# Kernel optimization log

Hardware: AMD Instinct MI355X
Metric: run time of the kernel (lower is better)

Reference implementation:

```python
import jax, jax.numpy as jnp
import numpy as np

N = 100000      # nodes
E = 400000      # edges
DIN, DH, DOUT = 32, 128, 1
EPS = 1e-5


def _lin_init(key, fan_in, shape):
    s = 1.0 / np.sqrt(fan_in)
    return jax.random.uniform(key, shape, jnp.float32, -s, s)


def setup_inputs() -> dict:
    key = jax.random.key(0)
    ks = jax.random.split(key, 24)
    x = jax.random.normal(ks[0], (N, DIN), jnp.float32)
    edge_index = jax.random.randint(ks[1], (2, E), 0, N, dtype=jnp.int64)
    d = {"x": x, "edge_index": edge_index}
    dims = [(DIN, DH), (DH, DH), (DH, DOUT)]
    for i, (din, dout) in enumerate(dims, start=1):
        d[f"W{i}"] = _lin_init(ks[2 * i], din, (din, dout))
        d[f"b{i}"] = _lin_init(ks[2 * i + 1], din, (dout,))
        d[f"g{i}"] = jnp.ones((dout,), jnp.float32)    # BatchNorm weight
        d[f"bt{i}"] = jnp.zeros((dout,), jnp.float32)  # BatchNorm bias
        d[f"lw{i}"] = jnp.ones((dout,), jnp.float32)   # LayerNorm weight
        d[f"lb{i}"] = jnp.zeros((dout,), jnp.float32)  # LayerNorm bias
    return d


def reference(x, edge_index, W1, b1, g1, bt1, lw1, lb1,
              W2, b2, g2, bt2, lw2, lb2,
              W3, b3, g3, bt3, lw3, lb3):
    n = x.shape[0]
    loop = jnp.arange(n, dtype=edge_index.dtype)
    src = jnp.concatenate([edge_index[0], loop])  # self-loops added (GCNConv default)
    dst = jnp.concatenate([edge_index[1], loop])
    deg = jax.ops.segment_sum(jnp.ones(src.shape[0], x.dtype), dst, num_segments=n)
    dinv = jnp.where(deg > 0, jax.lax.rsqrt(deg), 0.0)
    norm = dinv[src] * dinv[dst]  # D^{-1/2} (A+I) D^{-1/2} edge weights

    def gcn(h, W, b):
        h = h @ W
        agg = jax.ops.segment_sum(h[src] * norm[:, None], dst, num_segments=n)
        return agg + b

    def bn(h, g, b):  # BatchNorm1d, training-mode batch stats (biased var)
        m = h.mean(0)
        v = h.var(0)
        return (h - m) * jax.lax.rsqrt(v + EPS) * g + b

    def inorm(h):  # PyG InstanceNorm, single graph, affine=False
        m = h.mean(0)
        v = h.var(0)
        return (h - m) * jax.lax.rsqrt(v + EPS)

    def lnorm(h, w, b):  # PyG LayerNorm, mode='graph': stats over all nodes+channels
        m = h.mean()
        v = h.var()
        return (h - m) * jax.lax.rsqrt(v + EPS) * w + b

    h = jax.nn.relu(lnorm(inorm(bn(gcn(x, W1, b1), g1, bt1)), lw1, lb1))
    h = jax.nn.relu(lnorm(inorm(bn(gcn(h, W2, b2), g2, bt2)), lw2, lb2))
    h = lnorm(inorm(bn(gcn(h, W3, b3), g3, bt3)), lw3, lb3)
    return h.flatten()
```

## Files before the change

kernel.cpp:

```cpp
#include <hip/hip_runtime.h>
#include <cstddef>

#define EPS 1e-5f

typedef __attribute__((ext_vector_type(8))) short bf16x8;
typedef __attribute__((ext_vector_type(8))) unsigned short u16x8;
typedef __attribute__((ext_vector_type(4))) float f32x4;

__device__ inline short f2bf(float f) {
    union { float f; unsigned u; } v;
    v.f = f;
    unsigned r = v.u + 0x7fff + ((v.u >> 16) & 1);
    return (short)(r >> 16);
}
__device__ inline float bf2f(unsigned short s) {
    union { unsigned u; float f; } v;
    v.u = ((unsigned)s) << 16;
    return v.f;
}

__global__ void hist_kernel(const int* __restrict__ dst, int E, int* __restrict__ counts) {
    int i = blockIdx.x * blockDim.x + threadIdx.x;
    if (i < E) atomicAdd(&counts[dst[i]], 1);
}

__global__ __launch_bounds__(1024) void scan_part(const int* __restrict__ counts,
                                                  int* __restrict__ rowptr,
                                                  int* __restrict__ aux, int n) {
    __shared__ int sh[1024];
    int t = threadIdx.x;
    int g = blockIdx.x * 1024 + t;
    int v = (g < n) ? counts[g] : 0;
    sh[t] = v;
    __syncthreads();
    for (int off = 1; off < 1024; off <<= 1) {
        int add = (t >= off) ? sh[t - off] : 0;
        __syncthreads();
        sh[t] += add;
        __syncthreads();
    }
    if (g < n) rowptr[g] = sh[t] - v;
    if (t == 1023) aux[blockIdx.x] = sh[t];
}

__global__ __launch_bounds__(128) void scan_aux(int* __restrict__ aux, int B) {
    __shared__ int sh[128];
    int t = threadIdx.x;
    int v = (t < B) ? aux[t] : 0;
    sh[t] = v;
    __syncthreads();
    for (int off = 1; off < 128; off <<= 1) {
        int add = (t >= off) ? sh[t - off] : 0;
        __syncthreads();
        sh[t] += add;
        __syncthreads();
    }
    if (t < B) aux[t] = sh[t] - v;
}

__global__ void scan_add(int* __restrict__ rowptr, const int* __restrict__ aux,
                         const int* __restrict__ counts, int* __restrict__ cur,
                         float* __restrict__ dinv, int n, int E) {
    int g = blockIdx.x * blockDim.x + threadIdx.x;
    if (g < n) {
        int r = rowptr[g] + aux[g >> 10];
        rowptr[g] = r;
        cur[g] = r;
        dinv[g] = rsqrtf((float)counts[g] + 1.0f);
    }
    if (g == 0) rowptr[n] = E;
}

__global__ void fill_kernel(const int* __restrict__ src, const int* __restrict__ dst, int E,
                            int* __restrict__ cur, const float* __restrict__ dinv,
                            int* __restrict__ esrc, float* __restrict__ ewt) {
    int e = blockIdx.x * blockDim.x + threadIdx.x;
    if (e < E) {
        int d = dst[e];
        int s = src[e];
        int p = atomicAdd(&cur[d], 1);
        esrc[p] = s;
        ewt[p] = dinv[s] * dinv[d];
    }
}

__global__ void wt_all_kernel(const float* __restrict__ W1, const float* __restrict__ W2,
                              unsigned short* __restrict__ Wt1, unsigned short* __restrict__ Wt2) {
    int o = blockIdx.x * blockDim.x + threadIdx.x;
    if (o < 32 * 128) {
        int c = o / 32, k = o % 32;
        Wt1[o] = (unsigned short)f2bf(W1[(size_t)k * 128 + c]);
    } else if (o < 32 * 128 + 128 * 128) {
        int o2 = o - 32 * 128;
        int c = o2 / 128, k = o2 % 128;
        Wt2[o2] = (unsigned short)f2bf(W2[(size_t)k * 128 + c]);
    }
}

template <int K, bool NORM, bool STATS>
__global__ __launch_bounds__(256) void gemm_mfma(const unsigned short* __restrict__ hb,
                                                 const unsigned short* __restrict__ Wt,
                                                 const float* __restrict__ ss,
                                                 unsigned short* __restrict__ outb,
                                                 float* __restrict__ sums, int n) {
    int wid = (blockIdx.x * 256 + threadIdx.x) >> 6;
    int wv = (threadIdx.x >> 6);
    int lane = threadIdx.x & 63;
    int m = lane & 15;
    int qd = lane >> 4;
    int r0 = wid * 32;
    if (!STATS && r0 >= n) return;

    f32x4 acc[2][8];
#pragma unroll
    for (int rt = 0; rt < 2; rt++)
#pragma unroll
        for (int ct = 0; ct < 8; ct++) acc[rt][ct] = (f32x4){0.f, 0.f, 0.f, 0.f};

    if (r0 < n) {
#pragma unroll
        for (int q = 0; q < K / 32; q++) {
            int k0 = q * 32 + qd * 8;
            bf16x8 a[2];
#pragma unroll
            for (int rt = 0; rt < 2; rt++) {
                int r = r0 + rt * 16 + m;
                bf16x8 av = (bf16x8){0, 0, 0, 0, 0, 0, 0, 0};
                if (r < n) av = *(const bf16x8*)(hb + (size_t)r * K + k0);
                if (NORM) {
#pragma unroll
                    for (int j = 0; j < 8; j++) {
                        float f = bf2f((unsigned short)av[j]);
                        f = fmaxf(fmaf(f, ss[k0 + j], ss[K + k0 + j]), 0.f);
                        av[j] = f2bf(f);
                    }
                }
                a[rt] = av;
            }
#pragma unroll
            for (int ct = 0; ct < 8; ct++) {
                bf16x8 b = *(const bf16x8*)(Wt + (size_t)(ct * 16 + m) * K + k0);
                acc[0][ct] = __builtin_amdgcn_mfma_f32_16x16x32_bf16(a[0], b, acc[0][ct], 0, 0, 0);
                acc[1][ct] = __builtin_amdgcn_mfma_f32_16x16x32_bf16(a[1], b, acc[1][ct], 0, 0, 0);
            }
        }
#pragma unroll
        for (int rt = 0; rt < 2; rt++)
#pragma unroll
            for (int i = 0; i < 4; i++) {
                int r = r0 + rt * 16 + qd * 4 + i;
                if (r < n) {
#pragma unroll
                    for (int ct = 0; ct < 8; ct++)
                        outb[(size_t)r * 128 + ct * 16 + m] = (unsigned short)f2bf(acc[rt][ct][i]);
                }
            }
    }

    if (STATS) {
        __shared__ float ls[4][128], lq[4][128];
#pragma unroll
        for (int ct = 0; ct < 8; ct++) {
            float s = 0.f, q = 0.f;
#pragma unroll
            for (int rt = 0; rt < 2; rt++)
#pragma unroll
                for (int i = 0; i < 4; i++) {
                    float v = acc[rt][ct][i];
                    s += v;
                    q += v * v;
                }
            s += __shfl_xor(s, 16, 64);
            s += __shfl_xor(s, 32, 64);
            q += __shfl_xor(q, 16, 64);
            q += __shfl_xor(q, 32, 64);
            if (qd == 0) {
                ls[wv][ct * 16 + m] = s;
                lq[wv][ct * 16 + m] = q;
            }
        }
        __syncthreads();
        int t = threadIdx.x;
        if (t < 128) {
            atomicAdd(&sums[t], ls[0][t] + ls[1][t] + ls[2][t] + ls[3][t]);
        } else {
            int c = t - 128;
            atomicAdd(&sums[128 + c], lq[0][c] + lq[1][c] + lq[2][c] + lq[3][c]);
        }
    }
}

__global__ void gemv_norm_bf(const unsigned short* __restrict__ hb, const float* __restrict__ W,
                             const float* __restrict__ ss, float* __restrict__ out, int n) {
    int gid = blockIdx.x * blockDim.x + threadIdx.x;
    int wid = gid >> 6, lane = gid & 63;
    int nw = (gridDim.x * blockDim.x) >> 6;
    int c = lane * 2;
    float w0 = W[c], w1 = W[c + 1];
    float s0 = ss[c], s1 = ss[c + 1];
    float t0 = ss[128 + c], t1 = ss[128 + c + 1];
    for (int r = wid; r < n; r += nw) {
        ushort2 u = ((const ushort2*)(hb + (size_t)r * 128))[lane];
        float a = fmaxf(fmaf(bf2f(u.x), s0, t0), 0.f);
        float b = fmaxf(fmaf(bf2f(u.y), s1, t1), 0.f);
        float v = fmaf(a, w0, b * w1);
#pragma unroll
        for (int off = 32; off > 0; off >>= 1) v += __shfl_down(v, off, 64);
        if (lane == 0) out[r] = v;
    }
}

__global__ __launch_bounds__(256) void agg128_bf(const unsigned short* __restrict__ tmp,
                                                 const int* __restrict__ rowptr,
                                                 const int* __restrict__ esrc,
                                                 const float* __restrict__ ewt,
                                                 const float* __restrict__ dinv,
                                                 unsigned short* __restrict__ agg, int n) {
    int node = (blockIdx.x << 3) + (threadIdx.x >> 5);
    if (node >= n) return;
    int c4 = threadIdx.x & 31;
    float di = dinv[node];
    float d2 = di * di;
    ushort4 t = ((const ushort4*)tmp)[(size_t)node * 32 + c4];
    float a0 = bf2f(t.x) * d2, a1 = bf2f(t.y) * d2, a2 = bf2f(t.z) * d2, a3 = bf2f(t.w) * d2;
    int j = rowptr[node], je = rowptr[node + 1];
    for (; j + 8 <= je; j += 8) {
        int s[8];
        float w[8];
        ushort4 v[8];
#pragma unroll
        for (int k = 0; k < 8; k++) { s[k] = esrc[j + k]; w[k] = ewt[j + k]; }
#pragma unroll
        for (int k = 0; k < 8; k++) v[k] = ((const ushort4*)tmp)[(size_t)s[k] * 32 + c4];
#pragma unroll
        for (int k = 0; k < 8; k++) {
            a0 = fmaf(bf2f(v[k].x), w[k], a0);
            a1 = fmaf(bf2f(v[k].y), w[k], a1);
            a2 = fmaf(bf2f(v[k].z), w[k], a2);
            a3 = fmaf(bf2f(v[k].w), w[k], a3);
        }
    }
    if (j + 4 <= je) {
        int s[4];
        float w[4];
        ushort4 v[4];
#pragma unroll
        for (int k = 0; k < 4; k++) { s[k] = esrc[j + k]; w[k] = ewt[j + k]; }
#pragma unroll
        for (int k = 0; k < 4; k++) v[k] = ((const ushort4*)tmp)[(size_t)s[k] * 32 + c4];
#pragma unroll
        for (int k = 0; k < 4; k++) {
            a0 = fmaf(bf2f(v[k].x), w[k], a0);
            a1 = fmaf(bf2f(v[k].y), w[k], a1);
            a2 = fmaf(bf2f(v[k].z), w[k], a2);
            a3 = fmaf(bf2f(v[k].w), w[k], a3);
        }
        j += 4;
    }
    for (; j < je; j++) {
        int s = esrc[j];
        float w = ewt[j];
        ushort4 v = ((const ushort4*)tmp)[(size_t)s * 32 + c4];
        a0 = fmaf(bf2f(v.x), w, a0);
        a1 = fmaf(bf2f(v.y), w, a1);
        a2 = fmaf(bf2f(v.z), w, a2);
        a3 = fmaf(bf2f(v.w), w, a3);
    }
    ushort4 o;
    o.x = (unsigned short)f2bf(a0);
    o.y = (unsigned short)f2bf(a1);
    o.z = (unsigned short)f2bf(a2);
    o.w = (unsigned short)f2bf(a3);
    ((ushort4*)agg)[(size_t)node * 32 + c4] = o;
}

__global__ __launch_bounds__(256) void stats128_bf(const unsigned short* __restrict__ a,
                                                   float* __restrict__ sums, int n) {
    __shared__ float ls[16][128], lq[16][128];
    int t = threadIdx.x;
    int rg = t >> 4;
    int cg = t & 15;
    float s[8], q[8];
#pragma unroll
    for (int k = 0; k < 8; k++) { s[k] = 0.f; q[k] = 0.f; }
    for (int r = blockIdx.x * 16 + rg; r < n; r += gridDim.x * 16) {
        u16x8 v = *(const u16x8*)(a + (size_t)r * 128 + cg * 8);
#pragma unroll
        for (int k = 0; k < 8; k++) {
            float f = bf2f(v[k]);
            s[k] += f;
            q[k] = fmaf(f, f, q[k]);
        }
    }
#pragma unroll
    for (int k = 0; k < 8; k++) {
        ls[rg][cg * 8 + k] = s[k];
        lq[rg][cg * 8 + k] = q[k];
    }
    __syncthreads();
    if (t < 128) {
        float v = 0.f;
#pragma unroll
        for (int i = 0; i < 16; i++) v += ls[i][t];
        atomicAdd(&sums[t], v);
    } else {
        int c = t - 128;
        float v = 0.f;
#pragma unroll
        for (int i = 0; i < 16; i++) v += lq[i][c];
        atomicAdd(&sums[128 + c], v);
    }
}

__global__ __launch_bounds__(256) void agg32_f(const float* __restrict__ x,
                                               const int* __restrict__ rowptr,
                                               const int* __restrict__ esrc,
                                               const float* __restrict__ ewt,
                                               const float* __restrict__ dinv,
                                               unsigned short* __restrict__ xab, int n) {
    int g = threadIdx.x >> 3;
    int lane = threadIdx.x & 7;
    int node = blockIdx.x * 32 + g;
    if (node >= n) return;
    int co = lane << 2;
    float di = dinv[node];
    float d2 = di * di;
    float4 a = *(const float4*)(x + ((size_t)node << 5) + co);
    a.x *= d2; a.y *= d2; a.z *= d2; a.w *= d2;
    int j = rowptr[node], je = rowptr[node + 1];
    for (; j + 4 <= je; j += 4) {
        int s0 = esrc[j], s1 = esrc[j + 1], s2 = esrc[j + 2], s3 = esrc[j + 3];
        float w0 = ewt[j], w1 = ewt[j + 1], w2 = ewt[j + 2], w3 = ewt[j + 3];
        float4 v0 = *(const float4*)(x + ((size_t)s0 << 5) + co);
        float4 v1 = *(const float4*)(x + ((size_t)s1 << 5) + co);
        float4 v2 = *(const float4*)(x + ((size_t)s2 << 5) + co);
        float4 v3 = *(const float4*)(x + ((size_t)s3 << 5) + co);
        a.x = fmaf(v0.x, w0, a.x); a.y = fmaf(v0.y, w0, a.y);
        a.z = fmaf(v0.z, w0, a.z); a.w = fmaf(v0.w, w0, a.w);
        a.x = fmaf(v1.x, w1, a.x); a.y = fmaf(v1.y, w1, a.y);
        a.z = fmaf(v1.z, w1, a.z); a.w = fmaf(v1.w, w1, a.w);
        a.x = fmaf(v2.x, w2, a.x); a.y = fmaf(v2.y, w2, a.y);
        a.z = fmaf(v2.z, w2, a.z); a.w = fmaf(v2.w, w2, a.w);
        a.x = fmaf(v3.x, w3, a.x); a.y = fmaf(v3.y, w3, a.y);
        a.z = fmaf(v3.z, w3, a.z); a.w = fmaf(v3.w, w3, a.w);
    }
    for (; j < je; j++) {
        int s = esrc[j];
        float w = ewt[j];
        float4 v = *(const float4*)(x + ((size_t)s << 5) + co);
        a.x = fmaf(v.x, w, a.x); a.y = fmaf(v.y, w, a.y);
        a.z = fmaf(v.z, w, a.z); a.w = fmaf(v.w, w, a.w);
    }
    ushort4 o;
    o.x = (unsigned short)f2bf(a.x);
    o.y = (unsigned short)f2bf(a.y);
    o.z = (unsigned short)f2bf(a.z);
    o.w = (unsigned short)f2bf(a.w);
    ((ushort4*)(xab + ((size_t)node << 5)))[lane] = o;
}

__global__ void agg1_stats(const float* __restrict__ tmp, const int* __restrict__ rowptr,
                           const int* __restrict__ esrc, const float* __restrict__ ewt,
                           const float* __restrict__ dinv, float* __restrict__ out,
                           float* __restrict__ part, int n) {
    int i = blockIdx.x * blockDim.x + threadIdx.x;
    float acc = 0.f;
    if (i < n) {
        float di = dinv[i];
        acc = tmp[i] * di * di;
        int j = rowptr[i], je = rowptr[i + 1];
        for (; j + 4 <= je; j += 4) {
            int s0 = esrc[j], s1 = esrc[j + 1], s2 = esrc[j + 2], s3 = esrc[j + 3];
            float w0 = ewt[j], w1 = ewt[j + 1], w2 = ewt[j + 2], w3 = ewt[j + 3];
            float v0 = tmp[s0], v1 = tmp[s1], v2 = tmp[s2], v3 = tmp[s3];
            acc = fmaf(v0, w0, acc);
            acc = fmaf(v1, w1, acc);
            acc = fmaf(v2, w2, acc);
            acc = fmaf(v3, w3, acc);
        }
        for (; j < je; j++) acc = fmaf(tmp[esrc[j]], ewt[j], acc);
        out[i] = acc;
    }
    float s = acc, q = acc * acc;
#pragma unroll
    for (int off = 32; off > 0; off >>= 1) {
        s += __shfl_down(s, off, 64);
        q += __shfl_down(q, off, 64);
    }
    if ((threadIdx.x & 63) == 0) {
        int wgid = (blockIdx.x * blockDim.x + threadIdx.x) >> 6;
        part[2 * wgid] = s;
        part[2 * wgid + 1] = q;
    }
}

__global__ __launch_bounds__(256) void reduce_part(const float* __restrict__ part,
                                                   float* __restrict__ sums, int nw) {
    __shared__ float ls[256], lq[256];
    int t = threadIdx.x;
    float s = 0.f, q = 0.f;
    for (int i = t; i < nw; i += 256) {
        s += part[2 * i];
        q += part[2 * i + 1];
    }
    ls[t] = s;
    lq[t] = q;
    __syncthreads();
    for (int off = 128; off > 0; off >>= 1) {
        if (t < off) {
            ls[t] += ls[t + off];
            lq[t] += lq[t + off];
        }
        __syncthreads();
    }
    if (t == 0) {
        sums[0] = ls[0];
        sums[1] = lq[0];
    }
}

__global__ void apply1_kernel(const float* __restrict__ sums, const float* __restrict__ g,
                              const float* __restrict__ lw, const float* __restrict__ lb,
                              const float* __restrict__ a, float* __restrict__ out, int n) {
    int i = blockIdx.x * blockDim.x + threadIdx.x;
    if (i >= n) return;
    float m = sums[0] / n;
    float v = sums[1] / n - m * m;
    v = v < 0.f ? 0.f : v;
    float bs = rsqrtf(v + EPS) * g[0];
    float vz = v * bs * bs;
    float t = bs * rsqrtf(vz + EPS);
    float GV = v * t * t;
    float S = t * rsqrtf(GV + EPS) * lw[0];
    float T = lb[0] - m * S;
    out[i] = fmaf(a[i], S, T);
}

template <int C>
__global__ void finalize_kernel(const float* __restrict__ sums, const float* __restrict__ g,
                                const float* __restrict__ lw, const float* __restrict__ lb,
                                float* __restrict__ ss, int n) {
    __shared__ float vt2[C];
    int c = threadIdx.x;
    float m = sums[c] / n;
    float v = sums[C + c] / n - m * m;
    v = v < 0.f ? 0.f : v;
    float gc = g[c];
    float bs = rsqrtf(v + EPS) * gc;
    float vz = v * bs * bs;
    float t = bs * rsqrtf(vz + EPS);
    vt2[c] = v * t * t;
    __syncthreads();
    if (c == 0) {
        float gv = 0.f;
        for (int i = 0; i < C; i++) gv += vt2[i];
        vt2[0] = gv / C;
    }
    __syncthreads();
    float GV = vt2[0];
    float S = t * rsqrtf(GV + EPS) * lw[c];
    ss[c] = S;
    ss[C + c] = lb[c] - m * S;
}

extern "C" void kernel_launch(void* const* d_in, const int* in_sizes, int n_in,
                              void* d_out, int out_size, void* d_ws, size_t ws_size,
                              hipStream_t stream) {
    const float* x = (const float*)d_in[0];
    const int* ei = (const int*)d_in[1];
    int n = in_sizes[0] / 32;
    int E = in_sizes[1] / 2;
    const int* src = ei;
    const int* dstp = ei + E;
    const float* W1 = (const float*)d_in[2];
    const float* g1 = (const float*)d_in[4];
    const float* lw1 = (const float*)d_in[6];
    const float* lb1 = (const float*)d_in[7];
    const float* W2 = (const float*)d_in[8];
    const float* g2 = (const float*)d_in[10];
    const float* lw2 = (const float*)d_in[12];
    const float* lb2 = (const float*)d_in[13];
    const float* W3 = (const float*)d_in[14];
    const float* g3 = (const float*)d_in[16];
    const float* lw3 = (const float*)d_in[18];
    const float* lb3 = (const float*)d_in[19];
    float* out = (float*)d_out;

    char* p = (char*)d_ws;
    int* counts = (int*)p;             p += (size_t)n * 4;
    int* cur = (int*)p;                p += (size_t)n * 4;
    int* rowptr = (int*)p;             p += (size_t)(n + 4) * 4;
    int* aux = (int*)p;                p += 128 * 4;
    int* esrc = (int*)p;               p += (size_t)E * 4;
    float* ewt = (float*)p;            p += (size_t)E * 4;
    float* dinv = (float*)p;           p += (size_t)n * 4;
    unsigned short* Wt1 = (unsigned short*)p;  p += 128 * 32 * 2;
    unsigned short* Wt2 = (unsigned short*)p;  p += 128 * 128 * 2;
    unsigned short* xa = (unsigned short*)p;   p += (size_t)n * 32 * 2;
    unsigned short* h1 = (unsigned short*)p;   p += (size_t)n * 128 * 2;
    unsigned short* t2 = (unsigned short*)p;   p += (size_t)n * 128 * 2;
    unsigned short* a2 = (unsigned short*)p;   p += (size_t)n * 128 * 2;
    float* t3 = (float*)p;             p += (size_t)n * 4;
    float* a3 = (float*)p;             p += (size_t)n * 4;
    float* sums1 = (float*)p;          p += 256 * 4;
    float* sums2 = (float*)p;          p += 256 * 4;
    float* sums3 = (float*)p;          p += 4 * 4;
    float* ss1 = (float*)p;            p += 256 * 4;
    float* ss2 = (float*)p;            p += 256 * 4;
    float* part3 = (float*)p;          p += ((size_t)(n + 255) / 256) * 4 * 2 * 4;

    int B = (n + 1023) / 1024;

    hipMemsetAsync(counts, 0, (size_t)n * 4, stream);
    hipMemsetAsync(sums1, 0, 516 * 4, stream);
    hist_kernel<<<(E + 255) / 256, 256, 0, stream>>>(dstp, E, counts);
    scan_part<<<B, 1024, 0, stream>>>(counts, rowptr, aux, n);
    scan_aux<<<1, 128, 0, stream>>>(aux, B);
    scan_add<<<(n + 255) / 256, 256, 0, stream>>>(rowptr, aux, counts, cur, dinv, n, E);
    fill_kernel<<<(E + 255) / 256, 256, 0, stream>>>(src, dstp, E, cur, dinv, esrc, ewt);
    wt_all_kernel<<<(32 * 128 + 128 * 128 + 255) / 256, 256, 0, stream>>>(W1, W2, Wt1, Wt2);

    int mblk = ((n + 31) / 32 + 3) / 4;

    agg32_f<<<(n + 31) / 32, 256, 0, stream>>>(x, rowptr, esrc, ewt, dinv, xa, n);
    gemm_mfma<32, false, true><<<mblk, 256, 0, stream>>>(xa, Wt1, nullptr, h1, sums1, n);
    finalize_kernel<128><<<1, 128, 0, stream>>>(sums1, g1, lw1, lb1, ss1, n);

    gemm_mfma<128, true, false><<<mblk, 256, 0, stream>>>(h1, Wt2, ss1, t2, nullptr, n);
    agg128_bf<<<(n + 7) / 8, 256, 0, stream>>>(t2, rowptr, esrc, ewt, dinv, a2, n);
    stats128_bf<<<512, 256, 0, stream>>>(a2, sums2, n);
    finalize_kernel<128><<<1, 128, 0, stream>>>(sums2, g2, lw2, lb2, ss2, n);

    int ablk1 = (n + 255) / 256;
    gemv_norm_bf<<<1024, 256, 0, stream>>>(a2, W3, ss2, t3, n);
    agg1_stats<<<ablk1, 256, 0, stream>>>(t3, rowptr, esrc, ewt, dinv, a3, part3, n);
    reduce_part<<<1, 256, 0, stream>>>(part3, sums3, ablk1 * 4);
    apply1_kernel<<<(n + 255) / 256, 256, 0, stream>>>(sums3, g3, lw3, lb3, a3, out, n);
}
```

Before: 311.0 us.

## Fuse setup kernels, use decoupled-lookback scan, widen agg128 loads to 16B

```diff
diff --git a/kernel.cpp b/kernel.cpp
--- a/kernel.cpp
+++ b/kernel.cpp
@@ -19,17 +19,44 @@
     return v.f;
 }
 
+__global__ void prep_kernel(const float* __restrict__ W1, const float* __restrict__ W2,
+                            unsigned short* __restrict__ Wt1, unsigned short* __restrict__ Wt2,
+                            int* __restrict__ counts, float* __restrict__ sums,
+                            unsigned long long* __restrict__ state, int* __restrict__ ticket,
+                            int n) {
+    int o = blockIdx.x * blockDim.x + threadIdx.x;
+    if (o < n) counts[o] = 0;
+    if (o < 516) sums[o] = 0.f;
+    if (o < 128) state[o] = 0ULL;
+    if (o == 0) *ticket = 0;
+    if (o < 32 * 128) {
+        int c = o / 32, k = o % 32;
+        Wt1[o] = (unsigned short)f2bf(W1[(size_t)k * 128 + c]);
+    } else if (o < 32 * 128 + 128 * 128) {
+        int o2 = o - 32 * 128;
+        int c = o2 / 128, k = o2 % 128;
+        Wt2[o2] = (unsigned short)f2bf(W2[(size_t)k * 128 + c]);
+    }
+}
+
 __global__ void hist_kernel(const int* __restrict__ dst, int E, int* __restrict__ counts) {
     int i = blockIdx.x * blockDim.x + threadIdx.x;
     if (i < E) atomicAdd(&counts[dst[i]], 1);
 }
 
-__global__ __launch_bounds__(1024) void scan_part(const int* __restrict__ counts,
-                                                  int* __restrict__ rowptr,
-                                                  int* __restrict__ aux, int n) {
+__global__ __launch_bounds__(1024) void scan_lookback(const int* __restrict__ counts,
+                                                      int* __restrict__ rowptr,
+                                                      int* __restrict__ cur,
+                                                      float* __restrict__ dinv,
+                                                      unsigned long long* __restrict__ state,
+                                                      int* __restrict__ ticket, int n, int E) {
     __shared__ int sh[1024];
+    __shared__ int sbid, sexcl;
     int t = threadIdx.x;
-    int g = blockIdx.x * 1024 + t;
+    if (t == 0) sbid = atomicAdd(ticket, 1);
+    __syncthreads();
+    int bid = sbid;
+    int g = bid * 1024 + t;
     int v = (g < n) ? counts[g] : 0;
     sh[t] = v;
     __syncthreads();
@@ -39,31 +66,30 @@
         sh[t] += add;
         __syncthreads();
     }
-    if (g < n) rowptr[g] = sh[t] - v;
-    if (t == 1023) aux[blockIdx.x] = sh[t];
-}
-
-__global__ __launch_bounds__(128) void scan_aux(int* __restrict__ aux, int B) {
-    __shared__ int sh[128];
-    int t = threadIdx.x;
-    int v = (t < B) ? aux[t] : 0;
-    sh[t] = v;
-    __syncthreads();
-    for (int off = 1; off < 128; off <<= 1) {
-        int add = (t >= off) ? sh[t - off] : 0;
-        __syncthreads();
-        sh[t] += add;
-        __syncthreads();
-    }
-    if (t < B) aux[t] = sh[t] - v;
-}
-
-__global__ void scan_add(int* __restrict__ rowptr, const int* __restrict__ aux,
-                         const int* __restrict__ counts, int* __restrict__ cur,
-                         float* __restrict__ dinv, int n, int E) {
-    int g = blockIdx.x * blockDim.x + threadIdx.x;
+    int total = sh[1023];
+    if (t == 0) {
+        if (bid == 0) {
+            atomicExch(&state[0], (2ULL << 32) | (unsigned)total);
+            sexcl = 0;
+        } else {
+            atomicExch(&state[bid], (1ULL << 32) | (unsigned)total);
+            int excl = 0;
+            int j = bid - 1;
+            while (true) {
+                unsigned long long s;
+                do { s = atomicAdd(&state[j], 0ULL); } while ((s >> 32) == 0);
+                excl += (int)(s & 0xffffffffULL);
+                if ((s >> 32) == 2ULL) break;
+                j--;
+            }
+            atomicExch(&state[bid], (2ULL << 32) | (unsigned)(excl + total));
+            sexcl = excl;
+        }
+    }
+    __syncthreads();
+    int excl = sexcl;
     if (g < n) {
-        int r = rowptr[g] + aux[g >> 10];
+        int r = excl + sh[t] - v;
         rowptr[g] = r;
         cur[g] = r;
         dinv[g] = rsqrtf((float)counts[g] + 1.0f);
@@ -81,19 +107,6 @@
         int p = atomicAdd(&cur[d], 1);
         esrc[p] = s;
         ewt[p] = dinv[s] * dinv[d];
-    }
-}
-
-__global__ void wt_all_kernel(const float* __restrict__ W1, const float* __restrict__ W2,
-                              unsigned short* __restrict__ Wt1, unsigned short* __restrict__ Wt2) {
-    int o = blockIdx.x * blockDim.x + threadIdx.x;
-    if (o < 32 * 128) {
-        int c = o / 32, k = o % 32;
-        Wt1[o] = (unsigned short)f2bf(W1[(size_t)k * 128 + c]);
-    } else if (o < 32 * 128 + 128 * 128) {
-        int o2 = o - 32 * 128;
-        int c = o2 / 128, k = o2 % 128;
-        Wt2[o2] = (unsigned short)f2bf(W2[(size_t)k * 128 + c]);
     }
 }
 
@@ -216,62 +229,54 @@
                                                  const float* __restrict__ ewt,
                                                  const float* __restrict__ dinv,
                                                  unsigned short* __restrict__ agg, int n) {
-    int node = (blockIdx.x << 3) + (threadIdx.x >> 5);
+    int node = (blockIdx.x << 4) + (threadIdx.x >> 4);
     if (node >= n) return;
-    int c4 = threadIdx.x & 31;
+    int co = (threadIdx.x & 15) << 3;
     float di = dinv[node];
     float d2 = di * di;
-    ushort4 t = ((const ushort4*)tmp)[(size_t)node * 32 + c4];
-    float a0 = bf2f(t.x) * d2, a1 = bf2f(t.y) * d2, a2 = bf2f(t.z) * d2, a3 = bf2f(t.w) * d2;
+    u16x8 t = *(const u16x8*)(tmp + ((size_t)node << 7) + co);
+    float acc[8];
+#pragma unroll
+    for (int k = 0; k < 8; k++) acc[k] = bf2f(t[k]) * d2;
     int j = rowptr[node], je = rowptr[node + 1];
     for (; j + 8 <= je; j += 8) {
         int s[8];
         float w[8];
-        ushort4 v[8];
+        u16x8 v[8];
 #pragma unroll
         for (int k = 0; k < 8; k++) { s[k] = esrc[j + k]; w[k] = ewt[j + k]; }
 #pragma unroll
-        for (int k = 0; k < 8; k++) v[k] = ((const ushort4*)tmp)[(size_t)s[k] * 32 + c4];
-#pragma unroll
-        for (int k = 0; k < 8; k++) {
-            a0 = fmaf(bf2f(v[k].x), w[k], a0);
-            a1 = fmaf(bf2f(v[k].y), w[k], a1);
-            a2 = fmaf(bf2f(v[k].z), w[k], a2);
-            a3 = fmaf(bf2f(v[k].w), w[k], a3);
-        }
+        for (int k = 0; k < 8; k++) v[k] = *(const u16x8*)(tmp + ((size_t)s[k] << 7) + co);
+#pragma unroll
+        for (int k = 0; k < 8; k++)
+#pragma unroll
+            for (int c = 0; c < 8; c++) acc[c] = fmaf(bf2f(v[k][c]), w[k], acc[c]);
     }
     if (j + 4 <= je) {
         int s[4];
         float w[4];
-        ushort4 v[4];
+        u16x8 v[4];
 #pragma unroll
         for (int k = 0; k < 4; k++) { s[k] = esrc[j + k]; w[k] = ewt[j + k]; }
 #pragma unroll
-        for (int k = 0; k < 4; k++) v[k] = ((const ushort4*)tmp)[(size_t)s[k] * 32 + c4];
-#pragma unroll
-        for (int k = 0; k < 4; k++) {
-            a0 = fmaf(bf2f(v[k].x), w[k], a0);
-            a1 = fmaf(bf2f(v[k].y), w[k], a1);
-            a2 = fmaf(bf2f(v[k].z), w[k], a2);
-            a3 = fmaf(bf2f(v[k].w), w[k], a3);
-        }
+        for (int k = 0; k < 4; k++) v[k] = *(const u16x8*)(tmp + ((size_t)s[k] << 7) + co);
+#pragma unroll
+        for (int k = 0; k < 4; k++)
+#pragma unroll
+            for (int c = 0; c < 8; c++) acc[c] = fmaf(bf2f(v[k][c]), w[k], acc[c]);
         j += 4;
     }
     for (; j < je; j++) {
         int s = esrc[j];
         float w = ewt[j];
-        ushort4 v = ((const ushort4*)tmp)[(size_t)s * 32 + c4];
-        a0 = fmaf(bf2f(v.x), w, a0);
-        a1 = fmaf(bf2f(v.y), w, a1);
-        a2 = fmaf(bf2f(v.z), w, a2);
-        a3 = fmaf(bf2f(v.w), w, a3);
-    }
-    ushort4 o;
-    o.x = (unsigned short)f2bf(a0);
-    o.y = (unsigned short)f2bf(a1);
-    o.z = (unsigned short)f2bf(a2);
-    o.w = (unsigned short)f2bf(a3);
-    ((ushort4*)agg)[(size_t)node * 32 + c4] = o;
+        u16x8 v = *(const u16x8*)(tmp + ((size_t)s << 7) + co);
+#pragma unroll
+        for (int c = 0; c < 8; c++) acc[c] = fmaf(bf2f(v[c]), w, acc[c]);
+    }
+    u16x8 o;
+#pragma unroll
+    for (int k = 0; k < 8; k++) o[k] = (unsigned short)f2bf(acc[k]);
+    *(u16x8*)(agg + ((size_t)node << 7) + co) = o;
 }
 
 __global__ __launch_bounds__(256) void stats128_bf(const unsigned short* __restrict__ a,
@@ -490,7 +495,8 @@
     int* counts = (int*)p;             p += (size_t)n * 4;
     int* cur = (int*)p;                p += (size_t)n * 4;
     int* rowptr = (int*)p;             p += (size_t)(n + 4) * 4;
-    int* aux = (int*)p;                p += 128 * 4;
+    unsigned long long* state = (unsigned long long*)p;  p += 128 * 8;
+    int* ticket = (int*)p;             p += 4 * 4;
     int* esrc = (int*)p;               p += (size_t)E * 4;
     float* ewt = (float*)p;            p += (size_t)E * 4;
     float* dinv = (float*)p;           p += (size_t)n * 4;
@@ -511,14 +517,11 @@
 
     int B = (n + 1023) / 1024;
 
-    hipMemsetAsync(counts, 0, (size_t)n * 4, stream);
-    hipMemsetAsync(sums1, 0, 516 * 4, stream);
+    prep_kernel<<<(n + 255) / 256, 256, 0, stream>>>(W1, W2, Wt1, Wt2, counts, sums1,
+                                                     state, ticket, n);
     hist_kernel<<<(E + 255) / 256, 256, 0, stream>>>(dstp, E, counts);
-    scan_part<<<B, 1024, 0, stream>>>(counts, rowptr, aux, n);
-    scan_aux<<<1, 128, 0, stream>>>(aux, B);
-    scan_add<<<(n + 255) / 256, 256, 0, stream>>>(rowptr, aux, counts, cur, dinv, n, E);
+    scan_lookback<<<B, 1024, 0, stream>>>(counts, rowptr, cur, dinv, state, ticket, n, E);
     fill_kernel<<<(E + 255) / 256, 256, 0, stream>>>(src, dstp, E, cur, dinv, esrc, ewt);
-    wt_all_kernel<<<(32 * 128 + 128 * 128 + 255) / 256, 256, 0, stream>>>(W1, W2, Wt1, Wt2);
 
     int mblk = ((n + 31) / 32 + 3) / 4;
 
@@ -527,7 +530,7 @@
     finalize_kernel<128><<<1, 128, 0, stream>>>(sums1, g1, lw1, lb1, ss1, n);
 
     gemm_mfma<128, true, false><<<mblk, 256, 0, stream>>>(h1, Wt2, ss1, t2, nullptr, n);
-    agg128_bf<<<(n + 7) / 8, 256, 0, stream>>>(t2, rowptr, esrc, ewt, dinv, a2, n);
+    agg128_bf<<<(n + 15) / 16, 256, 0, stream>>>(t2, rowptr, esrc, ewt, dinv, a2, n);
     stats128_bf<<<512, 256, 0, stream>>>(a2, sums2, n);
     finalize_kernel<128><<<1, 128, 0, stream>>>(sums2, g2, lw2, lb2, ss2, n);
 
```

New measurement: 307.7 us. Within noise of the previous version (-1.1%).
